# Kernel tuning notes

Measured on AMD Instinct MI355X. Metric: run time of the kernel, lower is better.

Reference implementation:

```python
import jax, jax.numpy as jnp
import numpy as np

FS = 30.0        # sampling rate (Hz)
HIGH_PASS = 40.0 # BPM
LOW_PASS = 250.0 # BPM


def setup_inputs() -> dict:
    key = jax.random.key(0)
    k1, k2 = jax.random.split(key)
    B, N = 1024, 16384
    outputs = jax.random.normal(k1, (B, N), dtype=jnp.float32)
    # heart rates in BPM, within (high_pass, low_pass) band so slices are non-degenerate
    targets = 45.0 + 150.0 * jax.random.uniform(k2, (B, 1), dtype=jnp.float32)
    return {"outputs": outputs, "targets": targets}


def reference(outputs, targets):
    N = outputs.shape[-1]
    F = N // 2 + 1
    pulse_band = jnp.array([HIGH_PASS / 60.0, LOW_PASS / 60.0], dtype=jnp.float32)
    f = jnp.linspace(0.0, FS / 2.0, F, dtype=jnp.float32)  # [F]
    min_idx = jnp.argmin(jnp.abs(f - pulse_band[0]))
    max_idx = jnp.argmin(jnp.abs(f - pulse_band[1]))

    outputs = outputs.reshape(-1, N)
    if targets.shape[-1] != 1:
        targets = jnp.mean(targets, axis=-1, keepdims=True)
    t_hz = targets.reshape(-1) / 60.0  # [B] target frequency in Hz

    # rfft with norm='forward' divides by N, matching torch.fft.rfft(norm='forward')
    X = jnp.fft.rfft(outputs, axis=-1, norm='forward')  # [B, F] complex
    P1 = X.real ** 2 + X.imag ** 2                       # [B, F] power spectrum

    # per-sample index of the reference (ground-truth) frequency bin
    ref_idx = jnp.argmin(jnp.abs(f[None, :] - t_hz[:, None]), axis=-1)  # [B]

    # vectorized masked reduction replacing the per-sample python loop:
    # sum over [min_idx, ref_idx-1) U [ref_idx+2, max_idx)
    j = jnp.arange(F)
    ri = ref_idx[:, None]
    mask = ((j[None, :] >= min_idx) & (j[None, :] < ri - 1)) | \
           ((j[None, :] >= ri + 2) & (j[None, :] < max_idx))
    other_sum = jnp.sum(jnp.where(mask, P1, 0.0), axis=-1)              # [B]
    denom = (max_idx - min_idx - 3).astype(jnp.float32)
    other_avrg = other_sum / denom

    pulse_freq_amp = jnp.take_along_axis(P1, ref_idx[:, None], axis=-1)[:, 0]  # [B]
    snrs = 10.0 * jnp.log10(pulse_freq_amp / other_avrg)
    return -jnp.mean(snrs)
```

## Files before the change

kernel.cpp:

```cpp
#include <hip/hip_runtime.h>
#include <math.h>

#define THREADS 512
#define MHALF 8192
#define NREAL 16384
#define MIN_IDX 364
#define MAX_IDX 2276

__device__ __forceinline__ int br13(int x) {
    return (int)(__brev((unsigned)x) >> 19);
}

__device__ __forceinline__ int PHI(int i) {
    return i ^ (((i >> 5) & 15) << 1);
}

__device__ __forceinline__ float2 wtw(float f) {
    return make_float2(__builtin_amdgcn_cosf(f), -__builtin_amdgcn_sinf(f));
}

__device__ __forceinline__ float2 cmul(float2 a, float2 b) {
    return make_float2(a.x * b.x - a.y * b.y, a.x * b.y + a.y * b.x);
}

__device__ __forceinline__ void bfly(float2& a, float2& b, float2 tw) {
    float2 t = make_float2(a.x - b.x, a.y - b.y);
    a.x += b.x; a.y += b.y;
    b = cmul(t, tw);
}

__device__ __forceinline__ void fft_block16(float2 v[16], float2 W1)
{
    constexpr float C16x[8] = {1.f,  0.92387953251128674f,  0.70710678118654757f,  0.38268343236508978f,
                               0.f, -0.38268343236508978f, -0.70710678118654757f, -0.92387953251128674f};
    constexpr float C16y[8] = {0.f, -0.38268343236508978f, -0.70710678118654757f, -0.92387953251128674f,
                              -1.f, -0.92387953251128674f, -0.70710678118654757f, -0.38268343236508978f};
    constexpr float C8x[4] = {1.f,  0.70710678118654757f,  0.f, -0.70710678118654757f};
    constexpr float C8y[4] = {0.f, -0.70710678118654757f, -1.f, -0.70710678118654757f};

    float2 W2 = cmul(W1, W1), W4 = cmul(W2, W2), W8 = cmul(W4, W4);

    #pragma unroll
    for (int m = 0; m < 8; ++m) {
        float2 tw = cmul(W1, make_float2(C16x[m], C16y[m]));
        bfly(v[m], v[m + 8], tw);
    }
    #pragma unroll
    for (int g = 0; g < 2; ++g) {
        #pragma unroll
        for (int m = 0; m < 4; ++m) {
            float2 tw = cmul(W2, make_float2(C8x[m], C8y[m]));
            bfly(v[8 * g + m], v[8 * g + m + 4], tw);
        }
    }
    float2 W4i = make_float2(W4.y, -W4.x);
    #pragma unroll
    for (int g = 0; g < 4; ++g) {
        bfly(v[4 * g + 0], v[4 * g + 2], W4);
        bfly(v[4 * g + 1], v[4 * g + 3], W4i);
    }
    #pragma unroll
    for (int g = 0; g < 8; ++g)
        bfly(v[2 * g], v[2 * g + 1], W8);
}

__global__ __launch_bounds__(THREADS, 2)
void negsnr_row_kernel(const float* __restrict__ x,
                       const float* __restrict__ targets,
                       float* __restrict__ snr_out)
{
    __shared__ float2 cf[MHALF];
    const int row  = blockIdx.x;
    const int tid  = threadIdx.x;
    const int lane = tid & 63;
    const int wave = tid >> 6;

    const float2* xr = (const float2*)(x + (size_t)row * NREAL);
    float2 v[16];
    #pragma unroll
    for (int m = 0; m < 16; ++m) v[m] = xr[tid + 512 * m];

    const float step = 15.0f / 8192.0f;
    const float t_hz = targets[row] / 60.0f;
    int ri;
    {
        int kf = (int)floorf(t_hz * (8192.0f / 15.0f));
        float best = 1e30f; ri = 0;
        #pragma unroll
        for (int d = -1; d <= 2; ++d) {
            int k = min(max(kf + d, 0), 8192);
            float dist = fabsf((float)k * step - t_hz);
            if (dist < best) { best = dist; ri = k; }
        }
    }

    fft_block16(v, wtw((float)tid * (1.0f / 8192.0f)));
    #pragma unroll
    for (int m = 0; m < 16; ++m) cf[PHI(tid + 512 * m)] = v[m];
    __syncthreads();

    const int low5 = tid & 31;
    const int base2 = low5 + ((tid >> 5) << 9);
    #pragma unroll
    for (int m = 0; m < 16; ++m) v[m] = cf[PHI(base2 + 32 * m)];
    fft_block16(v, wtw((float)low5 * (1.0f / 512.0f)));
    #pragma unroll
    for (int m = 0; m < 16; ++m) cf[PHI(base2 + 32 * m)] = v[m];
    __syncthreads();

    const int p = tid & 1;
    const int base3 = p + ((tid >> 1) << 5);
    #pragma unroll
    for (int m = 0; m < 16; ++m) v[m] = cf[PHI(base3 + 2 * m)];
    {
        float2 U = p ? make_float2(0.98078528040323044f, -0.19509032201612825f)
                     : make_float2(1.0f, 0.0f);
        fft_block16(v, U);
    }
    #pragma unroll
    for (int m = 0; m < 16; ++m) cf[PHI(base3 + 2 * m)] = v[m];
    __syncthreads();

    float other = 0.0f, pulse = 0.0f;
    bool hasp = false;
    for (int k = MIN_IDX + tid; k < MAX_IDX; k += THREADS) {
        int a = br13(k);
        int b = br13(MHALF - k);
        float4 ya = *(const float4*)&cf[PHI(a)];
        float4 yb = *(const float4*)&cf[PHI(b - 1)];
        float Zr  = ya.x + ya.z, Zi  = ya.y + ya.w;
        float Zmr = yb.x - yb.z, Zmi = yb.y - yb.w;
        float xer  = 0.5f * (Zr + Zmr), xei = 0.5f * (Zi - Zmi);
        float xor_ = 0.5f * (Zi + Zmi), xoi = -0.5f * (Zr - Zmr);
        float2 tw = wtw((float)k * (1.0f / 16384.0f));
        float xr_ = xer + tw.x * xor_ - tw.y * xoi;
        float xi_ = xei + tw.x * xoi + tw.y * xor_;
        float pw = xr_ * xr_ + xi_ * xi_;
        if (k < ri - 1 || k > ri + 1) other += pw;
        if (k == ri) { pulse = pw; hasp = true; }
    }
    __syncthreads();
    if (hasp) cf[8].x = pulse;
    #pragma unroll
    for (int off = 32; off; off >>= 1) other += __shfl_down(other, off);
    if (lane == 0) cf[wave].x = other;
    __syncthreads();
    if (tid == 0) {
        float tot = 0.0f;
        #pragma unroll
        for (int w = 0; w < 8; ++w) tot += cf[w].x;
        const float denom = (float)(MAX_IDX - MIN_IDX - 3);
        snr_out[row] = 10.0f * log10f(cf[8].x * denom / tot);
    }
}

__global__ void negsnr_mean_kernel(const float* __restrict__ snr,
                                   float* __restrict__ out, int n)
{
    __shared__ float sacc[4];
    const int tid = threadIdx.x;
    float acc = 0.0f;
    for (int i = tid; i < n; i += 256) acc += snr[i];
    #pragma unroll
    for (int off = 32; off; off >>= 1) acc += __shfl_down(acc, off);
    if ((tid & 63) == 0) sacc[tid >> 6] = acc;
    __syncthreads();
    if (tid == 0) {
        float t = sacc[0] + sacc[1] + sacc[2] + sacc[3];
        out[0] = -t / (float)n;
    }
}

extern "C" void kernel_launch(void* const* d_in, const int* in_sizes, int n_in,
                              void* d_out, int out_size, void* d_ws, size_t ws_size,
                              hipStream_t stream) {
    const float* outputs = (const float*)d_in[0];
    const float* targets = (const float*)d_in[1];
    const int B = in_sizes[1];
    float* snr = (float*)d_ws;

    negsnr_row_kernel<<<B, THREADS, 0, stream>>>(outputs, targets, snr);
    negsnr_mean_kernel<<<1, 256, 0, stream>>>(snr, (float*)d_out, B);
}
```

Measured before the change: 37.45 us.

## Pack two real rows into one complex 16K FFT per block

Replaces the per-row half-length complex FFT (real-to-complex packing trick with a twiddle post-pass) with a two-for-one scheme: two real rows become the real and imaginary parts of one 16384-point complex FFT computed by a 1024-thread block. Each row's spectrum is then recovered from the conjugate-symmetric pair, which removes the post-processing twiddle multiplies. Work per block doubles, 64KB of LDS is used per block, and the grid is halved. This may limit occupancy and cut the number of concurrent blocks.

```diff
diff --git a/kernel.cpp b/kernel.cpp
--- a/kernel.cpp
+++ b/kernel.cpp
@@ -1,18 +1,17 @@
 #include <hip/hip_runtime.h>
 #include <math.h>
 
-#define THREADS 512
-#define MHALF 8192
-#define NREAL 16384
+#define THREADS 1024
+#define NFFT 16384
 #define MIN_IDX 364
 #define MAX_IDX 2276
 
-__device__ __forceinline__ int br13(int x) {
-    return (int)(__brev((unsigned)x) >> 19);
-}
-
-__device__ __forceinline__ int PHI(int i) {
-    return i ^ (((i >> 5) & 15) << 1);
+__device__ __forceinline__ int br12(int x) {
+    return (int)(__brev((unsigned)x) >> 20);
+}
+
+__device__ __forceinline__ int PHI(int p) {
+    return p ^ (((p >> 8) & 7) << 1);
 }
 
 __device__ __forceinline__ float2 wtw(float f) {
@@ -64,93 +63,113 @@
         bfly(v[2 * g], v[2 * g + 1], W8);
 }
 
-__global__ __launch_bounds__(THREADS, 2)
-void negsnr_row_kernel(const float* __restrict__ x,
-                       const float* __restrict__ targets,
-                       float* __restrict__ snr_out)
+__device__ __forceinline__ int ref_idx(float t_hz) {
+    const float step = 15.0f / 8192.0f;
+    int kf = (int)floorf(t_hz * (8192.0f / 15.0f));
+    int ri = 0; float best = 1e30f;
+    #pragma unroll
+    for (int d = -1; d <= 2; ++d) {
+        int k = min(max(kf + d, 0), 8192);
+        float dist = fabsf((float)k * step - t_hz);
+        if (dist < best) { best = dist; ri = k; }
+    }
+    return ri;
+}
+
+__global__ __launch_bounds__(THREADS, 4)
+void negsnr_pair_kernel(const float* __restrict__ x,
+                        const float* __restrict__ targets,
+                        float* __restrict__ snr_out)
 {
-    __shared__ float2 cf[MHALF];
-    const int row  = blockIdx.x;
+    __shared__ float2 cf[NFFT];
+    const int pair = blockIdx.x;
     const int tid  = threadIdx.x;
     const int lane = tid & 63;
     const int wave = tid >> 6;
 
-    const float2* xr = (const float2*)(x + (size_t)row * NREAL);
+    const float* ra = x + (size_t)(2 * pair) * NFFT;
+    const float* rb = ra + NFFT;
     float2 v[16];
     #pragma unroll
-    for (int m = 0; m < 16; ++m) v[m] = xr[tid + 512 * m];
-
-    const float step = 15.0f / 8192.0f;
-    const float t_hz = targets[row] / 60.0f;
-    int ri;
+    for (int m = 0; m < 16; ++m) {
+        v[m].x = ra[tid + 1024 * m];
+        v[m].y = rb[tid + 1024 * m];
+    }
+
+    const int riA = ref_idx(targets[2 * pair]     / 60.0f);
+    const int riB = ref_idx(targets[2 * pair + 1] / 60.0f);
+
+    fft_block16(v, wtw((float)tid * (1.0f / 16384.0f)));
+    #pragma unroll
+    for (int m = 0; m < 16; ++m) cf[PHI(tid + 1024 * m)] = v[m];
+    __syncthreads();
+
     {
-        int kf = (int)floorf(t_hz * (8192.0f / 15.0f));
-        float best = 1e30f; ri = 0;
-        #pragma unroll
-        for (int d = -1; d <= 2; ++d) {
-            int k = min(max(kf + d, 0), 8192);
-            float dist = fabsf((float)k * step - t_hz);
-            if (dist < best) { best = dist; ri = k; }
-        }
-    }
-
-    fft_block16(v, wtw((float)tid * (1.0f / 8192.0f)));
-    #pragma unroll
-    for (int m = 0; m < 16; ++m) cf[PHI(tid + 512 * m)] = v[m];
-    __syncthreads();
-
-    const int low5 = tid & 31;
-    const int base2 = low5 + ((tid >> 5) << 9);
-    #pragma unroll
-    for (int m = 0; m < 16; ++m) v[m] = cf[PHI(base2 + 32 * m)];
-    fft_block16(v, wtw((float)low5 * (1.0f / 512.0f)));
-    #pragma unroll
-    for (int m = 0; m < 16; ++m) cf[PHI(base2 + 32 * m)] = v[m];
-    __syncthreads();
-
-    const int p = tid & 1;
-    const int base3 = p + ((tid >> 1) << 5);
-    #pragma unroll
-    for (int m = 0; m < 16; ++m) v[m] = cf[PHI(base3 + 2 * m)];
+        const int q = tid & 63, base = q + ((tid >> 6) << 10);
+        #pragma unroll
+        for (int m = 0; m < 16; ++m) v[m] = cf[PHI(base + 64 * m)];
+        fft_block16(v, wtw((float)q * (1.0f / 1024.0f)));
+        #pragma unroll
+        for (int m = 0; m < 16; ++m) cf[PHI(base + 64 * m)] = v[m];
+    }
+    __syncthreads();
+
     {
-        float2 U = p ? make_float2(0.98078528040323044f, -0.19509032201612825f)
-                     : make_float2(1.0f, 0.0f);
-        fft_block16(v, U);
-    }
-    #pragma unroll
-    for (int m = 0; m < 16; ++m) cf[PHI(base3 + 2 * m)] = v[m];
-    __syncthreads();
-
-    float other = 0.0f, pulse = 0.0f;
-    bool hasp = false;
+        const int q2 = tid & 3, base = q2 + ((tid >> 2) << 6);
+        #pragma unroll
+        for (int m = 0; m < 16; ++m) v[m] = cf[PHI(base + 4 * m)];
+        fft_block16(v, wtw((float)q2 * (1.0f / 64.0f)));
+        #pragma unroll
+        for (int m = 0; m < 16; ++m) cf[PHI(base + 4 * m)] = v[m];
+    }
+    __syncthreads();
+
+    float oA = 0.0f, oB = 0.0f, pA = 0.0f, pB = 0.0f;
+    bool hA = false, hB = false;
     for (int k = MIN_IDX + tid; k < MAX_IDX; k += THREADS) {
-        int a = br13(k);
-        int b = br13(MHALF - k);
-        float4 ya = *(const float4*)&cf[PHI(a)];
-        float4 yb = *(const float4*)&cf[PHI(b - 1)];
-        float Zr  = ya.x + ya.z, Zi  = ya.y + ya.w;
-        float Zmr = yb.x - yb.z, Zmi = yb.y - yb.w;
-        float xer  = 0.5f * (Zr + Zmr), xei = 0.5f * (Zi - Zmi);
-        float xor_ = 0.5f * (Zi + Zmi), xoi = -0.5f * (Zr - Zmr);
-        float2 tw = wtw((float)k * (1.0f / 16384.0f));
-        float xr_ = xer + tw.x * xor_ - tw.y * xoi;
-        float xi_ = xei + tw.x * xoi + tw.y * xor_;
-        float pw = xr_ * xr_ + xi_ * xi_;
-        if (k < ri - 1 || k > ri + 1) other += pw;
-        if (k == ri) { pulse = pw; hasp = true; }
-    }
-    __syncthreads();
-    if (hasp) cf[8].x = pulse;
-    #pragma unroll
-    for (int off = 32; off; off >>= 1) other += __shfl_down(other, off);
-    if (lane == 0) cf[wave].x = other;
+        const int a  = br12(k);
+        const int a2 = br12(4096 - k);
+        const int s1 = ((a  >> 6) & 7) << 1;
+        const int s2 = ((a2 >> 6) & 7) << 1;
+        float4 u01 = *(const float4*)&cf[(4 * a)     ^ s1];
+        float4 u23 = *(const float4*)&cf[(4 * a + 2) ^ s1];
+        float4 w01 = *(const float4*)&cf[(4 * a2)     ^ s2];
+        float4 w23 = *(const float4*)&cf[(4 * a2 + 2) ^ s2];
+
+        float Zr = u01.x + u01.z + u23.x + u23.z;
+        float Zi = u01.y + u01.w + u23.y + u23.w;
+        float d02r = w01.x - w23.x, d02i = w01.y - w23.y;
+        float d13r = w01.z - w23.z, d13i = w01.w - w23.w;
+        float Zmr = d02r - d13i;
+        float Zmi = d02i + d13r;
+
+        float Ar = Zr + Zmr, Ai = Zi - Zmi;
+        float Br = Zr - Zmr, Bi = Zi + Zmi;
+        float PA = Ar * Ar + Ai * Ai;
+        float PB = Br * Br + Bi * Bi;
+
+        if (k < riA - 1 || k > riA + 1) oA += PA;
+        if (k == riA) { pA = PA; hA = true; }
+        if (k < riB - 1 || k > riB + 1) oB += PB;
+        if (k == riB) { pB = PB; hB = true; }
+    }
+    __syncthreads();
+    if (hA) cf[16].x = pA;
+    if (hB) cf[16].y = pB;
+    #pragma unroll
+    for (int off = 32; off; off >>= 1) {
+        oA += __shfl_down(oA, off);
+        oB += __shfl_down(oB, off);
+    }
+    if (lane == 0) { cf[wave].x = oA; cf[wave].y = oB; }
     __syncthreads();
     if (tid == 0) {
-        float tot = 0.0f;
-        #pragma unroll
-        for (int w = 0; w < 8; ++w) tot += cf[w].x;
+        float tA = 0.0f, tB = 0.0f;
+        #pragma unroll
+        for (int w = 0; w < 16; ++w) { tA += cf[w].x; tB += cf[w].y; }
         const float denom = (float)(MAX_IDX - MIN_IDX - 3);
-        snr_out[row] = 10.0f * log10f(cf[8].x * denom / tot);
+        snr_out[2 * pair]     = 10.0f * log10f(cf[16].x * denom / tA);
+        snr_out[2 * pair + 1] = 10.0f * log10f(cf[16].y * denom / tB);
     }
 }
 
@@ -179,6 +198,6 @@
     const int B = in_sizes[1];
     float* snr = (float*)d_ws;
 
-    negsnr_row_kernel<<<B, THREADS, 0, stream>>>(outputs, targets, snr);
+    negsnr_pair_kernel<<<B / 2, THREADS, 0, stream>>>(outputs, targets, snr);
     negsnr_mean_kernel<<<1, 256, 0, stream>>>(snr, (float*)d_out, B);
 }
```

New measurement: 40.39 us. 1.08x slower.
